# Kernel optimization log

Measured on AMD Instinct MI355X. Metric: run time of the kernel, lower is better.

## Reference

```python
import jax, jax.numpy as jnp
import numpy as np

B, C, H, W = 2, 64, 96, 96
DQK = C // 8  # query/key channel dim = 8


def setup_inputs() -> dict:
    key = jax.random.key(0)
    ks = jax.random.split(key, 8)
    s = 0.05
    x = jax.random.normal(ks[0], (B, C, H, W), dtype=jnp.float32)
    Wq = jax.random.normal(ks[1], (DQK, C), dtype=jnp.float32) * s
    bq = jax.random.normal(ks[2], (DQK,), dtype=jnp.float32) * s
    Wk = jax.random.normal(ks[3], (DQK, C), dtype=jnp.float32) * s
    bk = jax.random.normal(ks[4], (DQK,), dtype=jnp.float32) * s
    Wv = jax.random.normal(ks[5], (C, C), dtype=jnp.float32) * s
    bv = jax.random.normal(ks[6], (C,), dtype=jnp.float32) * s
    gamma = jax.random.normal(ks[7], (1,), dtype=jnp.float32) * s
    return {"x": x, "Wq": Wq, "bq": bq, "Wk": Wk, "bk": bk,
            "Wv": Wv, "bv": bv, "gamma": gamma}


def _attend(x, Wq, bq, Wk, bk, Wv, bv, gamma):
    b, c, h, w = x.shape
    p = h * w
    xf = x.reshape(b, c, p)                                    # [B,C,P]
    # 1x1 convs == per-pixel linear maps
    q = jnp.einsum('dc,bcp->bpd', Wq, xf) + bq                 # [B,P,d]
    k = jnp.einsum('dc,bcp->bdp', Wk, xf) + bk[None, :, None]  # [B,d,P]
    v = jnp.einsum('oc,bcp->bop', Wv, xf) + bv[None, :, None]  # [B,C,P]
    # energy[b,i,j] = q_i . k_j ; softmax over keys j (no 1/sqrt(d) scale,
    # matching the original module)
    energy = jnp.einsum('bpd,bdq->bpq', q, k)                  # [B,P,P]
    attn = jax.nn.softmax(energy, axis=-1)                     # [B,P,P]
    out = jnp.einsum('bcq,bpq->bcp', v, attn)                  # [B,C,P]
    out = out.reshape(b, c, h, w)
    return gamma * out + x


def reference(x, Wq, bq, Wk, bk, Wv, bv, gamma):
    return _attend(x, Wq, bq, Wk, bk, Wv, bv, gamma)
```

## Files before the change

kernel.cpp:

```cpp
#include <hip/hip_runtime.h>
#include <hip/hip_bf16.h>
#include <stdint.h>

#define BB 2
#define CC 64
#define PP 9216
#define QTILES 144
#define LOG2E 1.4426950408889634f
#define SCH_C 16248.664965f

typedef unsigned short ushort;
typedef __attribute__((ext_vector_type(8))) short short8;
typedef __attribute__((ext_vector_type(4))) float floatx4;
typedef __attribute__((ext_vector_type(4))) int intx4;

__device__ __forceinline__ ushort f2bf(float f) {
    unsigned int u = __float_as_uint(f);
    u = (u + 0x7fffu + ((u >> 16) & 1u)) >> 16;
    return (ushort)u;
}

__device__ __forceinline__ unsigned int exp2_pk_bf16(float e0, float e1) {
    const int i0 = (int)fmaf(e0, 128.f, SCH_C);
    const int i1 = (int)fmaf(e1, 128.f, SCH_C);
    return (unsigned int)i0 | ((unsigned int)i1 << 16);
}

__global__ __launch_bounds__(256)
void proj3(const float* __restrict__ x,
           const float* __restrict__ Wq, const float* __restrict__ bq,
           const float* __restrict__ Wk, const float* __restrict__ bk,
           const float* __restrict__ Wv, const float* __restrict__ bv,
           ushort* __restrict__ qbuf, ushort* __restrict__ kbuf,
           ushort* __restrict__ vfw)
{
    const int tid = threadIdx.x;
    const int px  = tid & 63;
    const int og  = __builtin_amdgcn_readfirstlane(tid >> 6);
    const int blk = blockIdx.x;
    const int b     = blk / (2 * QTILES);
    const int rem   = blk % (2 * QTILES);
    const int ptile = rem >> 1;
    const int rhalf = rem & 1;
    const int p     = ptile * 64 + px;
    const int r0    = rhalf * 40 + og * 10;

    const float* wr[10];
#pragma unroll
    for (int r = 0; r < 10; ++r) {
        const int row = r0 + r;
        wr[r] = (row < 8) ? (Wq + row * 64)
              : (row < 16) ? (Wk + (row - 8) * 64)
              : (Wv + (row - 16) * 64);
    }

    float xv[64];
#pragma unroll
    for (int c = 0; c < 64; ++c)
        xv[c] = x[((size_t)b * 64 + c) * PP + p];

    float acc[10];
#pragma unroll
    for (int r = 0; r < 10; ++r) acc[r] = 0.f;
#pragma unroll
    for (int c = 0; c < 64; ++c) {
#pragma unroll
        for (int r = 0; r < 10; ++r)
            acc[r] = fmaf(wr[r][c], xv[c], acc[r]);
    }

#pragma unroll
    for (int r = 0; r < 10; ++r) {
        const int row = r0 + r;
        if (row < 8) {
            const float v = (acc[r] + bq[row]) * LOG2E;
            qbuf[((size_t)b * PP + p) * 8 + row] = f2bf(v);
        } else if (row < 16) {
            const float v = acc[r] + bk[row - 8];
            kbuf[((size_t)b * PP + p) * 8 + (row - 8)] = f2bf(v);
        } else {
            const int co = row - 16;
            const float v = acc[r] + bv[co];
            const int pl = p & 31;
            const int ps = (p & ~31) | ((((pl >> 2) & 3) << 3) | (((pl >> 4) & 1) << 2) | (pl & 3));
            vfw[((size_t)b * 64 + co) * PP + ps] = f2bf(v);
        }
    }
}

__global__ __launch_bounds__(128, 3)
void attn7(const ushort* __restrict__ qbuf, const ushort* __restrict__ kbuf,
           const ushort* __restrict__ vfw,
           ushort* __restrict__ accp, float* __restrict__ lsump,
           int keysPerG, int numTiles)
{
    __shared__ __align__(16) float smerge[64 * 64];
    __shared__ float slsum[64];

    const int tid  = threadIdx.x;
    const int lane = tid & 63;
    const int wid  = tid >> 6;
    const int col  = lane & 15;
    const int quad = lane >> 4;

    const int qt = blockIdx.x % QTILES;
    const int gb = blockIdx.x / QTILES;
    const int b  = gb % BB;
    const int g  = gb / BB;
    const int q0 = qt * 64;

    const short8 zf = {0, 0, 0, 0, 0, 0, 0, 0};
    const short vone = (short)0x3F80;
    const short8 vones = {vone, vone, vone, vone, vone, vone, vone, vone};

    short8 qfragB[4];
#pragma unroll
    for (int qh = 0; qh < 4; ++qh)
        qfragB[qh] = (quad == 0)
            ? *(const short8*)(qbuf + ((size_t)b * PP + q0 + qh * 16 + col) * 8)
            : zf;

    floatx4 acc[4][4];
#pragma unroll
    for (int qh = 0; qh < 4; ++qh)
#pragma unroll
        for (int cb = 0; cb < 4; ++cb) acc[qh][cb] = (floatx4){0.f, 0.f, 0.f, 0.f};
    floatx4 accLh[4];
#pragma unroll
    for (int qh = 0; qh < 4; ++qh) accLh[qh] = (floatx4){0.f, 0.f, 0.f, 0.f};

    const ushort* kB = kbuf + (size_t)b * PP * 8;
    const ushort* vB = vfw + (size_t)b * 64 * PP;
    const int kwbase = g * keysPerG + wid * 32;

    short8 kf0c = *(const short8*)(kB + (size_t)(kwbase + col) * 8 + quad * 8);
    short8 kf1c = *(const short8*)(kB + (size_t)(kwbase + 16 + col) * 8 + quad * 8);
    short8 vfc[4];
#pragma unroll
    for (int cb = 0; cb < 4; ++cb)
        vfc[cb] = *(const short8*)(vB + ((size_t)(cb * 16 + col)) * PP + kwbase + quad * 8);

    for (int t = 0; t < numTiles; ++t) {
        const int tn  = (t + 1 < numTiles) ? (t + 1) : t;
        const int kwn = kwbase + tn * 64;

        const short8 kf0n = *(const short8*)(kB + (size_t)(kwn + col) * 8 + quad * 8);
        const short8 kf1n = *(const short8*)(kB + (size_t)(kwn + 16 + col) * 8 + quad * 8);
        short8 vfn[4];
#pragma unroll
        for (int cb = 0; cb < 4; ++cb)
            vfn[cb] = *(const short8*)(vB + ((size_t)(cb * 16 + col)) * PP + kwn + quad * 8);

#pragma unroll
        for (int qh = 0; qh < 4; ++qh) {
            const floatx4 E0 = __builtin_amdgcn_mfma_f32_16x16x32_bf16(
                kf0c, qfragB[qh], (floatx4){0.f, 0.f, 0.f, 0.f}, 0, 0, 0);
            const floatx4 E1 = __builtin_amdgcn_mfma_f32_16x16x32_bf16(
                kf1c, qfragB[qh], (floatx4){0.f, 0.f, 0.f, 0.f}, 0, 0, 0);

            intx4 pi;
            pi.x = (int)exp2_pk_bf16(E0[0], E0[1]);
            pi.y = (int)exp2_pk_bf16(E0[2], E0[3]);
            pi.z = (int)exp2_pk_bf16(E1[0], E1[1]);
            pi.w = (int)exp2_pk_bf16(E1[2], E1[3]);
            const short8 pf = __builtin_bit_cast(short8, pi);

            accLh[qh] = __builtin_amdgcn_mfma_f32_16x16x32_bf16(vones, pf, accLh[qh], 0, 0, 0);
#pragma unroll
            for (int cb = 0; cb < 4; ++cb)
                acc[qh][cb] = __builtin_amdgcn_mfma_f32_16x16x32_bf16(
                    vfc[cb], pf, acc[qh][cb], 0, 0, 0);
        }

        kf0c = kf0n;
        kf1c = kf1n;
#pragma unroll
        for (int cb = 0; cb < 4; ++cb) vfc[cb] = vfn[cb];
    }

    if (wid == 1) {
#pragma unroll
        for (int qh = 0; qh < 4; ++qh)
#pragma unroll
            for (int cb = 0; cb < 4; ++cb)
#pragma unroll
                for (int r = 0; r < 4; ++r)
                    smerge[(cb * 16 + quad * 4 + r) * 64 + qh * 16 + col] = acc[qh][cb][r];
        if (quad == 0)
#pragma unroll
            for (int qh = 0; qh < 4; ++qh)
                slsum[qh * 16 + col] = accLh[qh][0];
    }
    __syncthreads();
    if (wid == 0) {
        ushort* ab = accp + ((size_t)g * BB + b) * CC * PP;
#pragma unroll
        for (int qh = 0; qh < 4; ++qh)
#pragma unroll
            for (int cb = 0; cb < 4; ++cb)
#pragma unroll
                for (int r = 0; r < 4; ++r) {
                    const int c = cb * 16 + quad * 4 + r;
                    const float v = acc[qh][cb][r] + smerge[c * 64 + qh * 16 + col];
                    ab[(size_t)c * PP + q0 + qh * 16 + col] = f2bf(v);
                }
        if (quad == 0) {
            float* lb = lsump + ((size_t)g * BB + b) * PP + q0;
#pragma unroll
            for (int qh = 0; qh < 4; ++qh)
                lb[qh * 16 + col] = accLh[qh][0] + slsum[qh * 16 + col];
        }
    }
}

__global__ __launch_bounds__(256)
void combine(const ushort* __restrict__ accp, const float* __restrict__ lsump,
             const float* __restrict__ x, const float* __restrict__ gamma,
             float* __restrict__ out, int G)
{
    const size_t i8 = ((size_t)blockIdx.x * 256 + threadIdx.x) * 8;
    const int b = (int)(i8 / ((size_t)CC * PP));
    const int p = (int)(i8 % PP);
    const float gm = gamma[0];

    float asum[8] = {}, lst[8] = {};
    for (int g = 0; g < G; ++g) {
        const uint4 av = *(const uint4*)(accp + (size_t)g * (BB * CC * PP) + i8);
        const unsigned int u[4] = {av.x, av.y, av.z, av.w};
#pragma unroll
        for (int k = 0; k < 4; ++k) {
            asum[2 * k]     += __uint_as_float(u[k] << 16);
            asum[2 * k + 1] += __uint_as_float(u[k] & 0xffff0000u);
        }
        const float* lp = lsump + ((size_t)g * BB + b) * PP + p;
        const float4 l0 = *(const float4*)lp;
        const float4 l1 = *(const float4*)(lp + 4);
        lst[0] += l0.x; lst[1] += l0.y; lst[2] += l0.z; lst[3] += l0.w;
        lst[4] += l1.x; lst[5] += l1.y; lst[6] += l1.z; lst[7] += l1.w;
    }

    const float4 x0 = *(const float4*)(x + i8);
    const float4 x1 = *(const float4*)(x + i8 + 4);
    float o[8] = {x0.x, x0.y, x0.z, x0.w, x1.x, x1.y, x1.z, x1.w};
#pragma unroll
    for (int j = 0; j < 8; ++j)
        o[j] = fmaf(asum[j], gm / fmaxf(lst[j], 1e-30f), o[j]);
    *(float4*)(out + i8)     = make_float4(o[0], o[1], o[2], o[3]);
    *(float4*)(out + i8 + 4) = make_float4(o[4], o[5], o[6], o[7]);
}

extern "C" void kernel_launch(void* const* d_in, const int* in_sizes, int n_in,
                              void* d_out, int out_size, void* d_ws, size_t ws_size,
                              hipStream_t stream)
{
    const float* x     = (const float*)d_in[0];
    const float* Wq    = (const float*)d_in[1];
    const float* bq    = (const float*)d_in[2];
    const float* Wk    = (const float*)d_in[3];
    const float* bk    = (const float*)d_in[4];
    const float* Wv    = (const float*)d_in[5];
    const float* bv    = (const float*)d_in[6];
    const float* gamma = (const float*)d_in[7];
    float* out = (float*)d_out;

    const size_t nQK  = (size_t)BB * PP * 8;
    const size_t nV   = (size_t)BB * CC * PP;
    const size_t base = 2 * nQK * 2 + nV * 2;
    const size_t perG = nV * 2 + (size_t)BB * PP * 4;
    const int G = (ws_size >= base + 8 * perG) ? 8
                : (ws_size >= base + 6 * perG) ? 6
                : (ws_size >= base + 4 * perG) ? 4 : 2;
    const int keysPerG = PP / G;
    const int numTiles = keysPerG / 64;

    ushort* qbuf = (ushort*)d_ws;
    ushort* kbuf = qbuf + nQK;
    ushort* vfw  = kbuf + nQK;
    ushort* accp = vfw + nV;
    float* lsump = (float*)(accp + (size_t)G * nV);

    proj3<<<dim3(BB * 2 * QTILES), dim3(256), 0, stream>>>(
        x, Wq, bq, Wk, bk, Wv, bv, qbuf, kbuf, vfw);
    attn7<<<dim3(G * BB * QTILES), dim3(128), 0, stream>>>(
        qbuf, kbuf, vfw, accp, lsump, keysPerG, numTiles);
    combine<<<dim3(576), dim3(256), 0, stream>>>(
        accp, lsump, x, gamma, out, G);
}
```

Baseline: 139.8 us.

## Switch attention kernel to 32x32x16 MFMA with per-wave query tiles

The attention kernel now uses 32x32x16 bf16 MFMA instead of 16x16x32. Each wave owns 32 queries and walks all keys in its split, rather than each wave covering half the keys for 64 queries. This removes the LDS merge and the __syncthreads between the two waves. The V layout permutation in the projection is changed to match the new MFMA operand layout, and the loop is double-buffered by hand over 32-key tiles. The risk is that each wave now issues more K/V loads per query, and the loop has twice as many iterations.

```diff
diff --git a/kernel.cpp b/kernel.cpp
--- a/kernel.cpp
+++ b/kernel.cpp
@@ -10,9 +10,10 @@
 #define SCH_C 16248.664965f
 
 typedef unsigned short ushort;
-typedef __attribute__((ext_vector_type(8))) short short8;
-typedef __attribute__((ext_vector_type(4))) float floatx4;
-typedef __attribute__((ext_vector_type(4))) int intx4;
+typedef __attribute__((ext_vector_type(8)))  short short8;
+typedef __attribute__((ext_vector_type(4)))  float floatx4;
+typedef __attribute__((ext_vector_type(16))) float floatx16;
+typedef __attribute__((ext_vector_type(4)))  int intx4;
 
 __device__ __forceinline__ ushort f2bf(float f) {
     unsigned int u = __float_as_uint(f);
@@ -82,135 +83,106 @@
             const int co = row - 16;
             const float v = acc[r] + bv[co];
             const int pl = p & 31;
-            const int ps = (p & ~31) | ((((pl >> 2) & 3) << 3) | (((pl >> 4) & 1) << 2) | (pl & 3));
+            const int ps = (p & ~31) | (pl & 0x13) | ((pl & 4) << 1) | ((pl & 8) >> 1);
             vfw[((size_t)b * 64 + co) * PP + ps] = f2bf(v);
         }
     }
 }
 
+#define COMPUTE_TILE32(KF, Vc0b0, Vc0b1, Vc1b0, Vc1b1)                         \
+    {                                                                          \
+        const floatx16 E = __builtin_amdgcn_mfma_f32_32x32x16_bf16(            \
+            KF, qf, zero16, 0, 0, 0);                                          \
+        intx4 pi0, pi1;                                                        \
+        pi0.x = (int)exp2_pk_bf16(E[0],  E[1]);                                \
+        pi0.y = (int)exp2_pk_bf16(E[2],  E[3]);                                \
+        pi0.z = (int)exp2_pk_bf16(E[4],  E[5]);                                \
+        pi0.w = (int)exp2_pk_bf16(E[6],  E[7]);                                \
+        pi1.x = (int)exp2_pk_bf16(E[8],  E[9]);                                \
+        pi1.y = (int)exp2_pk_bf16(E[10], E[11]);                               \
+        pi1.z = (int)exp2_pk_bf16(E[12], E[13]);                               \
+        pi1.w = (int)exp2_pk_bf16(E[14], E[15]);                               \
+        const short8 pf0 = __builtin_bit_cast(short8, pi0);                    \
+        const short8 pf1 = __builtin_bit_cast(short8, pi1);                    \
+        accL = __builtin_amdgcn_mfma_f32_32x32x16_bf16(vones, pf0, accL, 0, 0, 0); \
+        accL = __builtin_amdgcn_mfma_f32_32x32x16_bf16(vones, pf1, accL, 0, 0, 0); \
+        acc0 = __builtin_amdgcn_mfma_f32_32x32x16_bf16(Vc0b0, pf0, acc0, 0, 0, 0); \
+        acc1 = __builtin_amdgcn_mfma_f32_32x32x16_bf16(Vc0b1, pf0, acc1, 0, 0, 0); \
+        acc0 = __builtin_amdgcn_mfma_f32_32x32x16_bf16(Vc1b0, pf1, acc0, 0, 0, 0); \
+        acc1 = __builtin_amdgcn_mfma_f32_32x32x16_bf16(Vc1b1, pf1, acc1, 0, 0, 0); \
+    }
+
 __global__ __launch_bounds__(128, 3)
-void attn7(const ushort* __restrict__ qbuf, const ushort* __restrict__ kbuf,
-           const ushort* __restrict__ vfw,
-           ushort* __restrict__ accp, float* __restrict__ lsump,
-           int keysPerG, int numTiles)
-{
-    __shared__ __align__(16) float smerge[64 * 64];
-    __shared__ float slsum[64];
-
+void attn11(const ushort* __restrict__ qbuf, const ushort* __restrict__ kbuf,
+            const ushort* __restrict__ vfw,
+            ushort* __restrict__ accp, float* __restrict__ lsump,
+            int keysPerG, int numTiles)
+{
     const int tid  = threadIdx.x;
     const int lane = tid & 63;
     const int wid  = tid >> 6;
-    const int col  = lane & 15;
-    const int quad = lane >> 4;
+    const int l31  = lane & 31;
+    const int hf   = lane >> 5;
 
     const int qt = blockIdx.x % QTILES;
     const int gb = blockIdx.x / QTILES;
     const int b  = gb % BB;
     const int g  = gb / BB;
-    const int q0 = qt * 64;
+    const int q0 = qt * 64 + wid * 32;
 
     const short8 zf = {0, 0, 0, 0, 0, 0, 0, 0};
     const short vone = (short)0x3F80;
     const short8 vones = {vone, vone, vone, vone, vone, vone, vone, vone};
-
-    short8 qfragB[4];
-#pragma unroll
-    for (int qh = 0; qh < 4; ++qh)
-        qfragB[qh] = (quad == 0)
-            ? *(const short8*)(qbuf + ((size_t)b * PP + q0 + qh * 16 + col) * 8)
-            : zf;
-
-    floatx4 acc[4][4];
-#pragma unroll
-    for (int qh = 0; qh < 4; ++qh)
-#pragma unroll
-        for (int cb = 0; cb < 4; ++cb) acc[qh][cb] = (floatx4){0.f, 0.f, 0.f, 0.f};
-    floatx4 accLh[4];
-#pragma unroll
-    for (int qh = 0; qh < 4; ++qh) accLh[qh] = (floatx4){0.f, 0.f, 0.f, 0.f};
+    const floatx16 zero16 = {0.f, 0.f, 0.f, 0.f, 0.f, 0.f, 0.f, 0.f,
+                             0.f, 0.f, 0.f, 0.f, 0.f, 0.f, 0.f, 0.f};
+
+    const short8 qf = (hf == 0)
+        ? *(const short8*)(qbuf + ((size_t)b * PP + q0 + l31) * 8)
+        : zf;
+
+    floatx16 acc0 = zero16;
+    floatx16 acc1 = zero16;
+    floatx16 accL = zero16;
 
     const ushort* kB = kbuf + (size_t)b * PP * 8;
     const ushort* vB = vfw + (size_t)b * 64 * PP;
-    const int kwbase = g * keysPerG + wid * 32;
-
-    short8 kf0c = *(const short8*)(kB + (size_t)(kwbase + col) * 8 + quad * 8);
-    short8 kf1c = *(const short8*)(kB + (size_t)(kwbase + 16 + col) * 8 + quad * 8);
-    short8 vfc[4];
-#pragma unroll
-    for (int cb = 0; cb < 4; ++cb)
-        vfc[cb] = *(const short8*)(vB + ((size_t)(cb * 16 + col)) * PP + kwbase + quad * 8);
-
-    for (int t = 0; t < numTiles; ++t) {
-        const int tn  = (t + 1 < numTiles) ? (t + 1) : t;
-        const int kwn = kwbase + tn * 64;
-
-        const short8 kf0n = *(const short8*)(kB + (size_t)(kwn + col) * 8 + quad * 8);
-        const short8 kf1n = *(const short8*)(kB + (size_t)(kwn + 16 + col) * 8 + quad * 8);
-        short8 vfn[4];
-#pragma unroll
-        for (int cb = 0; cb < 4; ++cb)
-            vfn[cb] = *(const short8*)(vB + ((size_t)(cb * 16 + col)) * PP + kwn + quad * 8);
-
-#pragma unroll
-        for (int qh = 0; qh < 4; ++qh) {
-            const floatx4 E0 = __builtin_amdgcn_mfma_f32_16x16x32_bf16(
-                kf0c, qfragB[qh], (floatx4){0.f, 0.f, 0.f, 0.f}, 0, 0, 0);
-            const floatx4 E1 = __builtin_amdgcn_mfma_f32_16x16x32_bf16(
-                kf1c, qfragB[qh], (floatx4){0.f, 0.f, 0.f, 0.f}, 0, 0, 0);
-
-            intx4 pi;
-            pi.x = (int)exp2_pk_bf16(E0[0], E0[1]);
-            pi.y = (int)exp2_pk_bf16(E0[2], E0[3]);
-            pi.z = (int)exp2_pk_bf16(E1[0], E1[1]);
-            pi.w = (int)exp2_pk_bf16(E1[2], E1[3]);
-            const short8 pf = __builtin_bit_cast(short8, pi);
-
-            accLh[qh] = __builtin_amdgcn_mfma_f32_16x16x32_bf16(vones, pf, accLh[qh], 0, 0, 0);
-#pragma unroll
-            for (int cb = 0; cb < 4; ++cb)
-                acc[qh][cb] = __builtin_amdgcn_mfma_f32_16x16x32_bf16(
-                    vfc[cb], pf, acc[qh][cb], 0, 0, 0);
-        }
-
-        kf0c = kf0n;
-        kf1c = kf1n;
-#pragma unroll
-        for (int cb = 0; cb < 4; ++cb) vfc[cb] = vfn[cb];
-    }
-
-    if (wid == 1) {
-#pragma unroll
-        for (int qh = 0; qh < 4; ++qh)
-#pragma unroll
-            for (int cb = 0; cb < 4; ++cb)
-#pragma unroll
-                for (int r = 0; r < 4; ++r)
-                    smerge[(cb * 16 + quad * 4 + r) * 64 + qh * 16 + col] = acc[qh][cb][r];
-        if (quad == 0)
-#pragma unroll
-            for (int qh = 0; qh < 4; ++qh)
-                slsum[qh * 16 + col] = accLh[qh][0];
-    }
-    __syncthreads();
-    if (wid == 0) {
-        ushort* ab = accp + ((size_t)g * BB + b) * CC * PP;
-#pragma unroll
-        for (int qh = 0; qh < 4; ++qh)
-#pragma unroll
-            for (int cb = 0; cb < 4; ++cb)
-#pragma unroll
-                for (int r = 0; r < 4; ++r) {
-                    const int c = cb * 16 + quad * 4 + r;
-                    const float v = acc[qh][cb][r] + smerge[c * 64 + qh * 16 + col];
-                    ab[(size_t)c * PP + q0 + qh * 16 + col] = f2bf(v);
-                }
-        if (quad == 0) {
-            float* lb = lsump + ((size_t)g * BB + b) * PP + q0;
-#pragma unroll
-            for (int qh = 0; qh < 4; ++qh)
-                lb[qh * 16 + col] = accLh[qh][0] + slsum[qh * 16 + col];
-        }
-    }
+    const int kwbase = g * keysPerG;
+
+    short8 kfa = *(const short8*)(kB + (size_t)(kwbase + l31) * 8);
+    short8 va00 = *(const short8*)(vB + ((size_t)(0 * 32 + l31)) * PP + kwbase + 0 * 16 + hf * 8);
+    short8 va01 = *(const short8*)(vB + ((size_t)(1 * 32 + l31)) * PP + kwbase + 0 * 16 + hf * 8);
+    short8 va10 = *(const short8*)(vB + ((size_t)(0 * 32 + l31)) * PP + kwbase + 1 * 16 + hf * 8);
+    short8 va11 = *(const short8*)(vB + ((size_t)(1 * 32 + l31)) * PP + kwbase + 1 * 16 + hf * 8);
+
+    for (int t = 0; t < numTiles; t += 2) {
+        const int kw1 = kwbase + (t + 1) * 32;
+        const short8 kfb  = *(const short8*)(kB + (size_t)(kw1 + l31) * 8);
+        const short8 vb00 = *(const short8*)(vB + ((size_t)(0 * 32 + l31)) * PP + kw1 + 0 * 16 + hf * 8);
+        const short8 vb01 = *(const short8*)(vB + ((size_t)(1 * 32 + l31)) * PP + kw1 + 0 * 16 + hf * 8);
+        const short8 vb10 = *(const short8*)(vB + ((size_t)(0 * 32 + l31)) * PP + kw1 + 1 * 16 + hf * 8);
+        const short8 vb11 = *(const short8*)(vB + ((size_t)(1 * 32 + l31)) * PP + kw1 + 1 * 16 + hf * 8);
+
+        COMPUTE_TILE32(kfa, va00, va01, va10, va11)
+
+        const int kw2 = (t + 2 < numTiles) ? (kwbase + (t + 2) * 32) : kw1;
+        kfa  = *(const short8*)(kB + (size_t)(kw2 + l31) * 8);
+        va00 = *(const short8*)(vB + ((size_t)(0 * 32 + l31)) * PP + kw2 + 0 * 16 + hf * 8);
+        va01 = *(const short8*)(vB + ((size_t)(1 * 32 + l31)) * PP + kw2 + 0 * 16 + hf * 8);
+        va10 = *(const short8*)(vB + ((size_t)(0 * 32 + l31)) * PP + kw2 + 1 * 16 + hf * 8);
+        va11 = *(const short8*)(vB + ((size_t)(1 * 32 + l31)) * PP + kw2 + 1 * 16 + hf * 8);
+
+        COMPUTE_TILE32(kfb, vb00, vb01, vb10, vb11)
+    }
+
+    ushort* ab = accp + ((size_t)g * BB + b) * CC * PP;
+#pragma unroll
+    for (int r = 0; r < 16; ++r) {
+        const int row = (r & 3) + 8 * (r >> 2) + 4 * hf;
+        ab[(size_t)row * PP + q0 + l31]        = f2bf(acc0[r]);
+        ab[(size_t)(32 + row) * PP + q0 + l31] = f2bf(acc1[r]);
+    }
+    if (lane < 32)
+        lsump[((size_t)g * BB + b) * PP + q0 + lane] = accL[0];
 }
 
 __global__ __launch_bounds__(256)
@@ -271,7 +243,7 @@
                 : (ws_size >= base + 6 * perG) ? 6
                 : (ws_size >= base + 4 * perG) ? 4 : 2;
     const int keysPerG = PP / G;
-    const int numTiles = keysPerG / 64;
+    const int numTiles = keysPerG / 32;
 
     ushort* qbuf = (ushort*)d_ws;
     ushort* kbuf = qbuf + nQK;
@@ -281,7 +253,7 @@
 
     proj3<<<dim3(BB * 2 * QTILES), dim3(256), 0, stream>>>(
         x, Wq, bq, Wk, bk, Wv, bv, qbuf, kbuf, vfw);
-    attn7<<<dim3(G * BB * QTILES), dim3(128), 0, stream>>>(
+    attn11<<<dim3(G * BB * QTILES), dim3(128), 0, stream>>>(
         qbuf, kbuf, vfw, accp, lsump, keysPerG, numTiles);
     combine<<<dim3(576), dim3(256), 0, stream>>>(
         accp, lsump, x, gamma, out, G);
```

Measured after the change: 172.4 us. +23.4%, slower.
